# Performance work log

Measured on AMD Instinct MI355X. Metric: run time of the kernel, lower is better.

## Reference

```python
import jax, jax.numpy as jnp
import numpy as np
from jax import lax

LN_EPS = 1e-5

def _expert_ffn_all(x, w1, b1, g_ln, b_ln, w2, b2):
    # x: [B,S,D]; w1: [E,D,F]; w2: [E,F,O]
    h = jnp.einsum('bsd,edf->bsef', x, w1) + b1[None, None]          # [B,S,E,F]
    h = jax.nn.gelu(h, approximate=False)                            # torch default GELU (erf)
    mu = jnp.mean(h, axis=-1, keepdims=True)
    var = jnp.var(h, axis=-1, keepdims=True)
    h = (h - mu) / jnp.sqrt(var + LN_EPS) * g_ln[None, None] + b_ln[None, None]
    return jnp.einsum('bsef,efo->bseo', h, w2) + b2[None, None]      # [B,S,E,O]

def _moe_forward(x, w_gate, w1, b1, g_ln, b_ln, w2, b2):
    B, S, D = x.shape
    E = w_gate.shape[1]
    k = max(1, S // E)  # capacity_factor=1.0
    logits = jnp.einsum('bsd,de->bse', x, w_gate)                    # x_gated [B,S,E]
    probs = jax.nn.softmax(logits, axis=-1)
    # expert-choice top-k along the sequence dim of the raw logits
    _, idx = lax.top_k(jnp.transpose(logits, (0, 2, 1)), k)          # [B,E,k]
    b_ix = jnp.arange(B)[:, None, None]
    e_ix = jnp.arange(E)[None, :, None]
    mask_t = jnp.zeros((B, E, S), dtype=probs.dtype).at[b_ix, e_ix, idx].set(1.0)
    gate_scores = probs * jnp.transpose(mask_t, (0, 2, 1))           # [B,S,E]
    expert_out = _expert_ffn_all(x, w1, b1, g_ln, b_ln, w2, b2)      # [B,S,E,O]
    moe_output = jnp.einsum('bse,bseo->bso', gate_scores, expert_out)
    return moe_output, logits

def setup_inputs() -> dict:
    key = jax.random.key(0)
    ks = jax.random.split(key, 4)
    B, S, D, F, O, E = 2, 2048, 1024, 2048, 1024, 8
    sc1 = 1.0 / np.sqrt(D)
    sc2 = 1.0 / np.sqrt(F)
    return {
        'x': jax.random.normal(ks[0], (B, S, D), jnp.float32),
        'w_gate': jax.random.normal(ks[1], (D, E), jnp.float32) * sc1,
        'w1': jax.random.normal(ks[2], (E, D, F), jnp.float32) * sc1,
        'b1': jnp.zeros((E, F), jnp.float32),
        'g_ln': jnp.ones((E, F), jnp.float32),
        'b_ln': jnp.zeros((E, F), jnp.float32),
        'w2': jax.random.normal(ks[3], (E, F, O), jnp.float32) * sc2,
        'b2': jnp.zeros((E, O), jnp.float32),
    }

def reference(x, w_gate, w1, b1, g_ln, b_ln, w2, b2):
    return _moe_forward(x, w_gate, w1, b1, g_ln, b_ln, w2, b2)
```

## Files before the change

kernel.cpp:

```cpp
#include <hip/hip_runtime.h>
#include <cstdint>
#include <cstddef>

typedef __attribute__((ext_vector_type(8))) short bf16x8;
typedef __attribute__((ext_vector_type(4))) float f32x4;

#define S_    2048
#define D_    1024
#define F_    2048
#define O_    1024
#define E_    8
#define KCAP  256
#define ROWS  512
#define NTOK  4096

#define BK 64

__device__ __forceinline__ unsigned short f2bf(float f) {
  unsigned int u = __float_as_uint(f);
  u = (u + 0x7fffu + ((u >> 16) & 1u)) >> 16;
  return (unsigned short)u;
}
__device__ __forceinline__ float bf2f(unsigned short h) {
  return __uint_as_float(((unsigned int)h) << 16);
}

__device__ __forceinline__ void gload16(void* lds, const void* g) {
  auto gp = (__attribute__((address_space(1))) unsigned int*)(uintptr_t)g;
  auto lp = (__attribute__((address_space(3))) unsigned int*)(unsigned int)(uintptr_t)lds;
  __builtin_amdgcn_global_load_lds(gp, lp, 16, 0, 0);
}

__global__ void gating_kernel(const float* __restrict__ x, const float* __restrict__ wg,
                              float* __restrict__ logits, float* __restrict__ probs,
                              unsigned short* __restrict__ xb) {
  const int wave = threadIdx.x >> 6, lane = threadIdx.x & 63;
  const int t = blockIdx.x * 4 + wave;
  const float* xr = x + (size_t)t * D_;
  double acc[8] = {0, 0, 0, 0, 0, 0, 0, 0};
  const int d0 = lane * 16;
#pragma unroll
  for (int i = 0; i < 4; i++) {
    float4 xv = *(const float4*)&xr[d0 + i * 4];
    union { ushort4 u4; unsigned short u[4]; } cv;
    cv.u[0] = f2bf(xv.x); cv.u[1] = f2bf(xv.y); cv.u[2] = f2bf(xv.z); cv.u[3] = f2bf(xv.w);
    *(ushort4*)&xb[(size_t)t * D_ + d0 + i * 4] = cv.u4;
    float xs[4] = {xv.x, xv.y, xv.z, xv.w};
#pragma unroll
    for (int j = 0; j < 4; j++) {
      const float4* wr = (const float4*)&wg[(size_t)(d0 + i * 4 + j) * 8];
      float4 w0 = wr[0], w1v = wr[1];
      double xd = (double)xs[j];
      acc[0] += xd * (double)w0.x;  acc[1] += xd * (double)w0.y;
      acc[2] += xd * (double)w0.z;  acc[3] += xd * (double)w0.w;
      acc[4] += xd * (double)w1v.x; acc[5] += xd * (double)w1v.y;
      acc[6] += xd * (double)w1v.z; acc[7] += xd * (double)w1v.w;
    }
  }
#pragma unroll
  for (int off = 32; off; off >>= 1) {
#pragma unroll
    for (int e = 0; e < 8; e++) acc[e] += __shfl_down(acc[e], off);
  }
  if (lane == 0) {
    double m = acc[0];
    for (int e = 1; e < 8; e++) m = acc[e] > m ? acc[e] : m;
    double p[8]; double s = 0;
    for (int e = 0; e < 8; e++) { p[e] = exp(acc[e] - m); s += p[e]; }
    const double inv = 1.0 / s;
    for (int e = 0; e < 8; e++) {
      logits[(size_t)t * 8 + e] = (float)acc[e];
      probs [(size_t)t * 8 + e] = (float)(p[e] * inv);
    }
  }
}

__global__ void transpose_cvt_kernel(const float* __restrict__ in, unsigned short* __restrict__ out,
                                     const int R, const int C) {
  __shared__ float t[64][65];
  const int e = blockIdx.z;
  const float* inp = in + (size_t)e * R * C;
  unsigned short* outp = out + (size_t)e * R * C;
  const int r0 = blockIdx.y * 64, c0 = blockIdx.x * 64;
  const int tid = threadIdx.x;
  const int lr = tid >> 4;
  const int lc = (tid & 15) * 4;
#pragma unroll
  for (int i = 0; i < 4; i++) {
    const int r = lr + i * 16;
    const float4 v = *(const float4*)&inp[(size_t)(r0 + r) * C + c0 + lc];
    t[r][lc] = v.x; t[r][lc + 1] = v.y; t[r][lc + 2] = v.z; t[r][lc + 3] = v.w;
  }
  __syncthreads();
#pragma unroll
  for (int i = 0; i < 4; i++) {
    const int oc = lr + i * 16;
    union { ushort4 u4; unsigned short u[4]; } u;
#pragma unroll
    for (int j = 0; j < 4; j++) u.u[j] = f2bf(t[lc + j][oc]);
    *(ushort4*)&outp[(size_t)(c0 + oc) * R + r0 + lc] = u.u4;
  }
}

__global__ void topk_kernel(const float* __restrict__ logits, const float* __restrict__ probs,
                            int* __restrict__ sel, float* __restrict__ gate) {
  __shared__ unsigned int keys[S_];
  const int idx = blockIdx.x;
  const int seg = idx & 7;
  const int be = idx >> 3;
  const int b = be >> 3;
  const int e = be & 7;
  const int tid = threadIdx.x;
  for (int i = tid; i < S_; i += 256) {
    unsigned int u = __float_as_uint(logits[((size_t)(b * S_ + i)) * E_ + e]);
    keys[i] = u ^ ((u & 0x80000000u) ? 0xFFFFFFFFu : 0x80000000u);
  }
  __syncthreads();
  const int s = seg * 256 + tid;
  const unsigned int vk = keys[s];
  const int wave = tid >> 6;
  const int W0 = seg * 256 + wave * 64;
  int rank = 0;
#pragma unroll 4
  for (int i = 0; i < W0; i += 4) {
    const uint4 kv = *(const uint4*)&keys[i];
    rank += (kv.x >= vk) + (kv.y >= vk) + (kv.z >= vk) + (kv.w >= vk);
  }
#pragma unroll
  for (int j = 0; j < 64; j++) {
    const int i = W0 + j;
    const unsigned int kv = keys[i];
    rank += (kv > vk) || (kv == vk && i < s);
  }
#pragma unroll 4
  for (int i = W0 + 64; i < S_; i += 4) {
    const uint4 kv = *(const uint4*)&keys[i];
    rank += (kv.x > vk) + (kv.y > vk) + (kv.z > vk) + (kv.w > vk);
  }
  if (rank < KCAP) {
    sel [e * ROWS + b * KCAP + rank] = b * S_ + s;
    gate[e * ROWS + b * KCAP + rank] = probs[((size_t)(b * S_ + s)) * E_ + e];
  }
}

__global__ __launch_bounds__(512, 4) void gemm1_kernel(
    const unsigned short* __restrict__ xb,
    const unsigned short* __restrict__ w1t,
    const float* __restrict__ b1,
    const int* __restrict__ sel,
    unsigned short* __restrict__ hbuf) {
  __shared__ unsigned short As[2][128 * 64];
  __shared__ unsigned short Bs[2][128 * 64];
  const int bid = blockIdx.x;
  const int lid = (bid & 7) * 64 + (bid >> 3);
  const int e   = lid >> 6;
  const int rem = lid & 63;
  const int m0  = (rem & 3) * 128;
  const int n0  = (rem >> 2) * 128;
  const int tid = threadIdx.x;
  const int wave = tid >> 6, lane = tid & 63;
  const int wrow = wave >> 2;
  const int wcol = wave & 3;

  const int srow = tid >> 3;
  const int schunk = ((tid & 7) ^ (srow & 7)) * 8;
  const unsigned short* a0 = xb + (size_t)sel[e * ROWS + m0 + srow] * D_ + schunk;
  const unsigned short* a1 = xb + (size_t)sel[e * ROWS + m0 + srow + 64] * D_ + schunk;
  const unsigned short* b0 = w1t + ((size_t)e * F_ + n0 + srow) * D_ + schunk;
  const unsigned short* b1p = w1t + ((size_t)e * F_ + n0 + srow + 64) * D_ + schunk;
  const int ldst0 = wave * 512;
  const int ldst1 = 4096 + wave * 512;

  f32x4 acc[4][2];
#pragma unroll
  for (int mi = 0; mi < 4; mi++)
#pragma unroll
    for (int nj = 0; nj < 2; nj++) acc[mi][nj] = (f32x4){0.f, 0.f, 0.f, 0.f};

  auto stage = [&](int buf, int t) {
    const int k0 = t * BK;
    gload16(&As[buf][ldst0], a0 + k0);
    gload16(&As[buf][ldst1], a1 + k0);
    gload16(&Bs[buf][ldst0], b0 + k0);
    gload16(&Bs[buf][ldst1], b1p + k0);
  };
  const int fr = lane & 15;
  auto compute = [&](int buf) {
    const unsigned short* Ab = As[buf];
    const unsigned short* Bb = Bs[buf];
#pragma unroll
    for (int kk = 0; kk < 2; kk++) {
      const int q = kk * 4 + (lane >> 4);
      bf16x8 a[4], b[2];
#pragma unroll
      for (int mi = 0; mi < 4; mi++) {
        const int r = wrow * 64 + mi * 16 + fr;
        a[mi] = *(const bf16x8*)&Ab[r * 64 + ((q ^ (r & 7)) * 8)];
      }
#pragma unroll
      for (int nj = 0; nj < 2; nj++) {
        const int r = wcol * 32 + nj * 16 + fr;
        b[nj] = *(const bf16x8*)&Bb[r * 64 + ((q ^ (r & 7)) * 8)];
      }
#pragma unroll
      for (int mi = 0; mi < 4; mi++)
#pragma unroll
        for (int nj = 0; nj < 2; nj++)
          acc[mi][nj] = __builtin_amdgcn_mfma_f32_16x16x32_bf16(a[mi], b[nj], acc[mi][nj], 0, 0, 0);
    }
  };

  const int NT = D_ / BK;
  stage(0, 0);
  stage(1, 1);
  for (int t = 0; t < NT; t++) {
    if (t < NT - 1) asm volatile("s_waitcnt vmcnt(4)" ::: "memory");
    else            asm volatile("s_waitcnt vmcnt(0)" ::: "memory");
    asm volatile("s_barrier" ::: "memory");
    compute(t & 1);
    if (t + 2 < NT) {
      asm volatile("s_barrier" ::: "memory");
      stage(t & 1, t + 2);
    }
  }

#pragma unroll
  for (int mi = 0; mi < 4; mi++)
#pragma unroll
    for (int nj = 0; nj < 2; nj++)
#pragma unroll
      for (int rg = 0; rg < 4; rg++) {
        const int row = m0 + wrow * 64 + mi * 16 + (lane >> 4) * 4 + rg;
        const int col = n0 + wcol * 32 + nj * 16 + fr;
        float v = acc[mi][nj][rg] + b1[e * F_ + col];
        v = 0.5f * v * (1.0f + erff(v * 0.70710678118654752f));
        hbuf[((size_t)e * ROWS + row) * F_ + col] = f2bf(v);
      }
}

__global__ void ln_kernel(unsigned short* __restrict__ hbuf,
                          const float* __restrict__ g_ln, const float* __restrict__ b_ln) {
  const int row = blockIdx.x;
  const int e = row >> 9;
  unsigned short* hr = hbuf + (size_t)row * F_;
  const int tid = threadIdx.x;
  union { bf16x8 v; unsigned short u[8]; } u;
  u.v = *(const bf16x8*)&hr[tid * 8];
  float vals[8]; float s1 = 0.f, s2 = 0.f;
#pragma unroll
  for (int j = 0; j < 8; j++) { float f = bf2f(u.u[j]); vals[j] = f; s1 += f; s2 += f * f; }
#pragma unroll
  for (int off = 32; off; off >>= 1) { s1 += __shfl_down(s1, off); s2 += __shfl_down(s2, off); }
  __shared__ float rs[8];
  const int wave = tid >> 6, lane = tid & 63;
  if (lane == 0) { rs[wave] = s1; rs[wave + 4] = s2; }
  __syncthreads();
  const float t1 = rs[0] + rs[1] + rs[2] + rs[3];
  const float t2 = rs[4] + rs[5] + rs[6] + rs[7];
  const float mu = t1 * (1.f / F_);
  const float var = t2 * (1.f / F_) - mu * mu;
  const float rstd = rsqrtf(var + 1e-5f);
  const float4* gl4 = (const float4*)(g_ln + (size_t)e * F_ + tid * 8);
  const float4* bl4 = (const float4*)(b_ln + (size_t)e * F_ + tid * 8);
  float4 g0 = gl4[0], g1 = gl4[1], bb0 = bl4[0], bb1 = bl4[1];
  float gs[8] = {g0.x, g0.y, g0.z, g0.w, g1.x, g1.y, g1.z, g1.w};
  float bs[8] = {bb0.x, bb0.y, bb0.z, bb0.w, bb1.x, bb1.y, bb1.z, bb1.w};
  union { bf16x8 v; unsigned short u[8]; } o;
#pragma unroll
  for (int j = 0; j < 8; j++)
    o.u[j] = f2bf((vals[j] - mu) * rstd * gs[j] + bs[j]);
  *(bf16x8*)&hr[tid * 8] = o.v;
}

__global__ __launch_bounds__(512, 4) void gemm2_kernel(
    const unsigned short* __restrict__ hbuf,
    const unsigned short* __restrict__ w2t,
    const float* __restrict__ b2,
    const int* __restrict__ sel, const float* __restrict__ gate,
    float* __restrict__ out) {
  __shared__ unsigned short As[2][128 * 64];
  __shared__ unsigned short Bs[2][128 * 64];
  const int bid = blockIdx.x;
  const int lid = (bid & 7) * 64 + (bid >> 3);
  const int e   = lid >> 6;
  const int rem = lid & 63;
  const int khalf = rem & 1;
  const int m0  = ((rem >> 1) & 3) * 128;
  const int n0  = (rem >> 3) * 128;
  const int koff = khalf * (F_ / 2);
  const int tid = threadIdx.x;
  const int wave = tid >> 6, lane = tid & 63;
  const int wrow = wave >> 2;
  const int wcol = wave & 3;

  const int srow = tid >> 3;
  const int schunk = ((tid & 7) ^ (srow & 7)) * 8;
  const unsigned short* a0 = hbuf + ((size_t)e * ROWS + m0 + srow) * F_ + koff + schunk;
  const unsigned short* a1 = hbuf + ((size_t)e * ROWS + m0 + srow + 64) * F_ + koff + schunk;
  const unsigned short* b0 = w2t + ((size_t)e * O_ + n0 + srow) * F_ + koff + schunk;
  const unsigned short* b1p = w2t + ((size_t)e * O_ + n0 + srow + 64) * F_ + koff + schunk;
  const int ldst0 = wave * 512;
  const int ldst1 = 4096 + wave * 512;

  f32x4 acc[4][2];
#pragma unroll
  for (int mi = 0; mi < 4; mi++)
#pragma unroll
    for (int nj = 0; nj < 2; nj++) acc[mi][nj] = (f32x4){0.f, 0.f, 0.f, 0.f};

  auto stage = [&](int buf, int t) {
    const int k0 = t * BK;
    gload16(&As[buf][ldst0], a0 + k0);
    gload16(&As[buf][ldst1], a1 + k0);
    gload16(&Bs[buf][ldst0], b0 + k0);
    gload16(&Bs[buf][ldst1], b1p + k0);
  };
  const int fr = lane & 15;
  auto compute = [&](int buf) {
    const unsigned short* Ab = As[buf];
    const unsigned short* Bb = Bs[buf];
#pragma unroll
    for (int kk = 0; kk < 2; kk++) {
      const int q = kk * 4 + (lane >> 4);
      bf16x8 a[4], b[2];
#pragma unroll
      for (int mi = 0; mi < 4; mi++) {
        const int r = wrow * 64 + mi * 16 + fr;
        a[mi] = *(const bf16x8*)&Ab[r * 64 + ((q ^ (r & 7)) * 8)];
      }
#pragma unroll
      for (int nj = 0; nj < 2; nj++) {
        const int r = wcol * 32 + nj * 16 + fr;
        b[nj] = *(const bf16x8*)&Bb[r * 64 + ((q ^ (r & 7)) * 8)];
      }
#pragma unroll
      for (int mi = 0; mi < 4; mi++)
#pragma unroll
        for (int nj = 0; nj < 2; nj++)
          acc[mi][nj] = __builtin_amdgcn_mfma_f32_16x16x32_bf16(a[mi], b[nj], acc[mi][nj], 0, 0, 0);
    }
  };

  const int NT = (F_ / 2) / BK;
  stage(0, 0);
  stage(1, 1);
  for (int t = 0; t < NT; t++) {
    if (t < NT - 1) asm volatile("s_waitcnt vmcnt(4)" ::: "memory");
    else            asm volatile("s_waitcnt vmcnt(0)" ::: "memory");
    asm volatile("s_barrier" ::: "memory");
    compute(t & 1);
    if (t + 2 < NT) {
      asm volatile("s_barrier" ::: "memory");
      stage(t & 1, t + 2);
    }
  }

#pragma unroll
  for (int mi = 0; mi < 4; mi++) {
#pragma unroll
    for (int rg = 0; rg < 4; rg++) {
      const int row = m0 + wrow * 64 + mi * 16 + (lane >> 4) * 4 + rg;
      const int tok = sel[e * ROWS + row];
      const float g = gate[e * ROWS + row];
#pragma unroll
      for (int nj = 0; nj < 2; nj++) {
        const int col = n0 + wcol * 32 + nj * 16 + fr;
        float v = acc[mi][nj][rg];
        if (khalf == 0) v += b2[e * O_ + col];
        atomicAdd(&out[(size_t)tok * O_ + col], g * v);
      }
    }
  }
}

extern "C" void kernel_launch(void* const* d_in, const int* in_sizes, int n_in,
                              void* d_out, int out_size, void* d_ws, size_t ws_size,
                              hipStream_t stream) {
  const float* x     = (const float*)d_in[0];
  const float* wg    = (const float*)d_in[1];
  const float* w1    = (const float*)d_in[2];
  const float* b1    = (const float*)d_in[3];
  const float* g_ln  = (const float*)d_in[4];
  const float* b_ln  = (const float*)d_in[5];
  const float* w2    = (const float*)d_in[6];
  const float* b2    = (const float*)d_in[7];
  float* out = (float*)d_out;
  float* out_logits = out + (size_t)NTOK * O_;

  char* wsb = (char*)d_ws;
  unsigned short* xb   = (unsigned short*)(wsb + 0);
  unsigned short* w1t  = (unsigned short*)(wsb + 8388608);
  unsigned short* w2t  = (unsigned short*)(wsb + 41943040);
  unsigned short* hbuf = (unsigned short*)(wsb + 75497472);
  float* probs = (float*)(wsb + 92274688);
  int*   sel   = (int*)  (wsb + 92405760);
  float* gate  = (float*)(wsb + 92422144);

  hipMemsetAsync(d_out, 0, (size_t)NTOK * O_ * sizeof(float), stream);

  gating_kernel<<<NTOK / 4, 256, 0, stream>>>(x, wg, out_logits, probs, xb);
  transpose_cvt_kernel<<<dim3(F_ / 64, D_ / 64, E_), 256, 0, stream>>>(w1, w1t, D_, F_);
  transpose_cvt_kernel<<<dim3(O_ / 64, F_ / 64, E_), 256, 0, stream>>>(w2, w2t, F_, O_);
  topk_kernel<<<2 * E_ * 8, 256, 0, stream>>>(out_logits, probs, sel, gate);
  gemm1_kernel<<<512, 512, 0, stream>>>(xb, w1t, b1, sel, hbuf);
  ln_kernel<<<E_ * ROWS, 256, 0, stream>>>(hbuf, g_ln, b_ln);
  gemm2_kernel<<<512, 512, 0, stream>>>(hbuf, w2t, b2, sel, gate, out);
}
```

Baseline: 162.7 us.

## Load GEMM B operand directly into registers and shrink tiles to 64x128

```diff
diff --git a/kernel.cpp b/kernel.cpp
--- a/kernel.cpp
+++ b/kernel.cpp
@@ -143,33 +143,32 @@
   }
 }
 
-__global__ __launch_bounds__(512, 4) void gemm1_kernel(
+__global__ __launch_bounds__(256, 4) void gemm1_kernel(
     const unsigned short* __restrict__ xb,
     const unsigned short* __restrict__ w1t,
     const float* __restrict__ b1,
     const int* __restrict__ sel,
     unsigned short* __restrict__ hbuf) {
-  __shared__ unsigned short As[2][128 * 64];
-  __shared__ unsigned short Bs[2][128 * 64];
+  __shared__ unsigned short As[2][64 * 64];
   const int bid = blockIdx.x;
-  const int lid = (bid & 7) * 64 + (bid >> 3);
-  const int e   = lid >> 6;
-  const int rem = lid & 63;
-  const int m0  = (rem & 3) * 128;
-  const int n0  = (rem >> 2) * 128;
+  const int lid = (bid & 7) * 128 + (bid >> 3);
+  const int e   = lid >> 7;
+  const int rem = lid & 127;
+  const int m0  = (rem & 7) * 64;
+  const int n0  = (rem >> 3) * 128;
   const int tid = threadIdx.x;
   const int wave = tid >> 6, lane = tid & 63;
-  const int wrow = wave >> 2;
-  const int wcol = wave & 3;
-
-  const int srow = tid >> 3;
-  const int schunk = ((tid & 7) ^ (srow & 7)) * 8;
-  const unsigned short* a0 = xb + (size_t)sel[e * ROWS + m0 + srow] * D_ + schunk;
-  const unsigned short* a1 = xb + (size_t)sel[e * ROWS + m0 + srow + 64] * D_ + schunk;
-  const unsigned short* b0 = w1t + ((size_t)e * F_ + n0 + srow) * D_ + schunk;
-  const unsigned short* b1p = w1t + ((size_t)e * F_ + n0 + srow + 64) * D_ + schunk;
-  const int ldst0 = wave * 512;
-  const int ldst1 = 4096 + wave * 512;
+  const int fr = lane & 15;
+  const int kq = lane >> 4;
+
+  const unsigned short* a_src[2];
+#pragma unroll
+  for (int j = 0; j < 2; j++) {
+    const int r = wave * 16 + j * 8 + (lane >> 3);
+    const int chunk = (lane & 7) ^ (r & 7);
+    a_src[j] = xb + (size_t)sel[e * ROWS + m0 + r] * D_ + chunk * 8;
+  }
+  const unsigned short* bptr = w1t + ((size_t)(e * F_ + n0 + wave * 32 + fr)) * D_ + kq * 8;
 
   f32x4 acc[4][2];
 #pragma unroll
@@ -177,50 +176,54 @@
 #pragma unroll
     for (int nj = 0; nj < 2; nj++) acc[mi][nj] = (f32x4){0.f, 0.f, 0.f, 0.f};
 
-  auto stage = [&](int buf, int t) {
+  bf16x8 breg[2][2][2];
+
+  auto stageA = [&](int buf, int t) {
     const int k0 = t * BK;
-    gload16(&As[buf][ldst0], a0 + k0);
-    gload16(&As[buf][ldst1], a1 + k0);
-    gload16(&Bs[buf][ldst0], b0 + k0);
-    gload16(&Bs[buf][ldst1], b1p + k0);
-  };
-  const int fr = lane & 15;
-  auto compute = [&](int buf) {
-    const unsigned short* Ab = As[buf];
-    const unsigned short* Bb = Bs[buf];
+    gload16(&As[buf][(wave * 16 + 0) * 64], a_src[0] + k0);
+    gload16(&As[buf][(wave * 16 + 8) * 64], a_src[1] + k0);
+  };
+  auto loadB = [&](int buf, int t) {
+    const size_t k0 = (size_t)t * BK;
+#pragma unroll
+    for (int kk = 0; kk < 2; kk++)
+#pragma unroll
+      for (int nj = 0; nj < 2; nj++)
+        breg[buf][kk][nj] = *(const bf16x8*)(bptr + (size_t)nj * 16 * D_ + k0 + kk * 32);
+  };
+  auto compute = [&](int abuf, int bbuf) {
+    const unsigned short* Ab = As[abuf];
 #pragma unroll
     for (int kk = 0; kk < 2; kk++) {
-      const int q = kk * 4 + (lane >> 4);
-      bf16x8 a[4], b[2];
+      const int q = kk * 4 + kq;
+      bf16x8 a[4];
 #pragma unroll
       for (int mi = 0; mi < 4; mi++) {
-        const int r = wrow * 64 + mi * 16 + fr;
+        const int r = mi * 16 + fr;
         a[mi] = *(const bf16x8*)&Ab[r * 64 + ((q ^ (r & 7)) * 8)];
       }
 #pragma unroll
-      for (int nj = 0; nj < 2; nj++) {
-        const int r = wcol * 32 + nj * 16 + fr;
-        b[nj] = *(const bf16x8*)&Bb[r * 64 + ((q ^ (r & 7)) * 8)];
-      }
-#pragma unroll
       for (int mi = 0; mi < 4; mi++)
 #pragma unroll
         for (int nj = 0; nj < 2; nj++)
-          acc[mi][nj] = __builtin_amdgcn_mfma_f32_16x16x32_bf16(a[mi], b[nj], acc[mi][nj], 0, 0, 0);
+          acc[mi][nj] = __builtin_amdgcn_mfma_f32_16x16x32_bf16(a[mi], breg[bbuf][kk][nj], acc[mi][nj], 0, 0, 0);
     }
   };
 
   const int NT = D_ / BK;
-  stage(0, 0);
-  stage(1, 1);
+  stageA(0, 0);
+  stageA(1, 1);
+  loadB(0, 0);
+#pragma unroll 2
   for (int t = 0; t < NT; t++) {
-    if (t < NT - 1) asm volatile("s_waitcnt vmcnt(4)" ::: "memory");
-    else            asm volatile("s_waitcnt vmcnt(0)" ::: "memory");
+    if (t + 1 < NT) loadB((t + 1) & 1, t + 1);
+    if (t < NT - 1) asm volatile("s_waitcnt vmcnt(10)" ::: "memory");
+    else            asm volatile("s_waitcnt vmcnt(4)"  ::: "memory");
     asm volatile("s_barrier" ::: "memory");
-    compute(t & 1);
+    compute(t & 1, t & 1);
     if (t + 2 < NT) {
       asm volatile("s_barrier" ::: "memory");
-      stage(t & 1, t + 2);
+      stageA(t & 1, t + 2);
     }
   }
 
@@ -230,8 +233,8 @@
     for (int nj = 0; nj < 2; nj++)
 #pragma unroll
       for (int rg = 0; rg < 4; rg++) {
-        const int row = m0 + wrow * 64 + mi * 16 + (lane >> 4) * 4 + rg;
-        const int col = n0 + wcol * 32 + nj * 16 + fr;
+        const int row = m0 + mi * 16 + (lane >> 4) * 4 + rg;
+        const int col = n0 + wave * 32 + nj * 16 + fr;
         float v = acc[mi][nj][rg] + b1[e * F_ + col];
         v = 0.5f * v * (1.0f + erff(v * 0.70710678118654752f));
         hbuf[((size_t)e * ROWS + row) * F_ + col] = f2bf(v);
@@ -272,35 +275,34 @@
   *(bf16x8*)&hr[tid * 8] = o.v;
 }
 
-__global__ __launch_bounds__(512, 4) void gemm2_kernel(
+__global__ __launch_bounds__(256, 4) void gemm2_kernel(
     const unsigned short* __restrict__ hbuf,
     const unsigned short* __restrict__ w2t,
     const float* __restrict__ b2,
     const int* __restrict__ sel, const float* __restrict__ gate,
     float* __restrict__ out) {
-  __shared__ unsigned short As[2][128 * 64];
-  __shared__ unsigned short Bs[2][128 * 64];
+  __shared__ unsigned short As[2][64 * 64];
   const int bid = blockIdx.x;
-  const int lid = (bid & 7) * 64 + (bid >> 3);
-  const int e   = lid >> 6;
-  const int rem = lid & 63;
-  const int khalf = rem & 1;
-  const int m0  = ((rem >> 1) & 3) * 128;
-  const int n0  = (rem >> 3) * 128;
-  const int koff = khalf * (F_ / 2);
+  const int lid = (bid & 7) * 128 + (bid >> 3);
+  const int e     = lid >> 7;
+  const int rem   = lid & 127;
+  const int m0    = (rem & 7) * 64;
+  const int n0    = ((rem >> 3) & 7) * 128;
+  const int khalf = (rem >> 6) & 1;
+  const int koff  = khalf * (F_ / 2);
   const int tid = threadIdx.x;
   const int wave = tid >> 6, lane = tid & 63;
-  const int wrow = wave >> 2;
-  const int wcol = wave & 3;
-
-  const int srow = tid >> 3;
-  const int schunk = ((tid & 7) ^ (srow & 7)) * 8;
-  const unsigned short* a0 = hbuf + ((size_t)e * ROWS + m0 + srow) * F_ + koff + schunk;
-  const unsigned short* a1 = hbuf + ((size_t)e * ROWS + m0 + srow + 64) * F_ + koff + schunk;
-  const unsigned short* b0 = w2t + ((size_t)e * O_ + n0 + srow) * F_ + koff + schunk;
-  const unsigned short* b1p = w2t + ((size_t)e * O_ + n0 + srow + 64) * F_ + koff + schunk;
-  const int ldst0 = wave * 512;
-  const int ldst1 = 4096 + wave * 512;
+  const int fr = lane & 15;
+  const int kq = lane >> 4;
+
+  const unsigned short* a_src[2];
+#pragma unroll
+  for (int j = 0; j < 2; j++) {
+    const int r = wave * 16 + j * 8 + (lane >> 3);
+    const int chunk = (lane & 7) ^ (r & 7);
+    a_src[j] = hbuf + ((size_t)e * ROWS + m0 + r) * F_ + koff + chunk * 8;
+  }
+  const unsigned short* bptr = w2t + ((size_t)(e * O_ + n0 + wave * 32 + fr)) * F_ + koff + kq * 8;
 
   f32x4 acc[4][2];
 #pragma unroll
@@ -308,50 +310,54 @@
 #pragma unroll
     for (int nj = 0; nj < 2; nj++) acc[mi][nj] = (f32x4){0.f, 0.f, 0.f, 0.f};
 
-  auto stage = [&](int buf, int t) {
+  bf16x8 breg[2][2][2];
+
+  auto stageA = [&](int buf, int t) {
     const int k0 = t * BK;
-    gload16(&As[buf][ldst0], a0 + k0);
-    gload16(&As[buf][ldst1], a1 + k0);
-    gload16(&Bs[buf][ldst0], b0 + k0);
-    gload16(&Bs[buf][ldst1], b1p + k0);
-  };
-  const int fr = lane & 15;
-  auto compute = [&](int buf) {
-    const unsigned short* Ab = As[buf];
-    const unsigned short* Bb = Bs[buf];
+    gload16(&As[buf][(wave * 16 + 0) * 64], a_src[0] + k0);
+    gload16(&As[buf][(wave * 16 + 8) * 64], a_src[1] + k0);
+  };
+  auto loadB = [&](int buf, int t) {
+    const size_t k0 = (size_t)t * BK;
+#pragma unroll
+    for (int kk = 0; kk < 2; kk++)
+#pragma unroll
+      for (int nj = 0; nj < 2; nj++)
+        breg[buf][kk][nj] = *(const bf16x8*)(bptr + (size_t)nj * 16 * F_ + k0 + kk * 32);
+  };
+  auto compute = [&](int abuf, int bbuf) {
+    const unsigned short* Ab = As[abuf];
 #pragma unroll
     for (int kk = 0; kk < 2; kk++) {
-      const int q = kk * 4 + (lane >> 4);
-      bf16x8 a[4], b[2];
+      const int q = kk * 4 + kq;
+      bf16x8 a[4];
 #pragma unroll
       for (int mi = 0; mi < 4; mi++) {
-        const int r = wrow * 64 + mi * 16 + fr;
+        const int r = mi * 16 + fr;
         a[mi] = *(const bf16x8*)&Ab[r * 64 + ((q ^ (r & 7)) * 8)];
       }
 #pragma unroll
-      for (int nj = 0; nj < 2; nj++) {
-        const int r = wcol * 32 + nj * 16 + fr;
-        b[nj] = *(const bf16x8*)&Bb[r * 64 + ((q ^ (r & 7)) * 8)];
-      }
-#pragma unroll
       for (int mi = 0; mi < 4; mi++)
 #pragma unroll
         for (int nj = 0; nj < 2; nj++)
-          acc[mi][nj] = __builtin_amdgcn_mfma_f32_16x16x32_bf16(a[mi], b[nj], acc[mi][nj], 0, 0, 0);
+          acc[mi][nj] = __builtin_amdgcn_mfma_f32_16x16x32_bf16(a[mi], breg[bbuf][kk][nj], acc[mi][nj], 0, 0, 0);
     }
   };
 
   const int NT = (F_ / 2) / BK;
-  stage(0, 0);
-  stage(1, 1);
+  stageA(0, 0);
+  stageA(1, 1);
+  loadB(0, 0);
+#pragma unroll 2
   for (int t = 0; t < NT; t++) {
-    if (t < NT - 1) asm volatile("s_waitcnt vmcnt(4)" ::: "memory");
-    else            asm volatile("s_waitcnt vmcnt(0)" ::: "memory");
+    if (t + 1 < NT) loadB((t + 1) & 1, t + 1);
+    if (t < NT - 1) asm volatile("s_waitcnt vmcnt(10)" ::: "memory");
+    else            asm volatile("s_waitcnt vmcnt(4)"  ::: "memory");
     asm volatile("s_barrier" ::: "memory");
-    compute(t & 1);
+    compute(t & 1, t & 1);
     if (t + 2 < NT) {
       asm volatile("s_barrier" ::: "memory");
-      stage(t & 1, t + 2);
+      stageA(t & 1, t + 2);
     }
   }
 
@@ -359,12 +365,12 @@
   for (int mi = 0; mi < 4; mi++) {
 #pragma unroll
     for (int rg = 0; rg < 4; rg++) {
-      const int row = m0 + wrow * 64 + mi * 16 + (lane >> 4) * 4 + rg;
+      const int row = m0 + mi * 16 + (lane >> 4) * 4 + rg;
       const int tok = sel[e * ROWS + row];
       const float g = gate[e * ROWS + row];
 #pragma unroll
       for (int nj = 0; nj < 2; nj++) {
-        const int col = n0 + wcol * 32 + nj * 16 + fr;
+        const int col = n0 + wave * 32 + nj * 16 + fr;
         float v = acc[mi][nj][rg];
         if (khalf == 0) v += b2[e * O_ + col];
         atomicAdd(&out[(size_t)tok * O_ + col], g * v);
@@ -402,7 +408,7 @@
   transpose_cvt_kernel<<<dim3(F_ / 64, D_ / 64, E_), 256, 0, stream>>>(w1, w1t, D_, F_);
   transpose_cvt_kernel<<<dim3(O_ / 64, F_ / 64, E_), 256, 0, stream>>>(w2, w2t, F_, O_);
   topk_kernel<<<2 * E_ * 8, 256, 0, stream>>>(out_logits, probs, sel, gate);
-  gemm1_kernel<<<512, 512, 0, stream>>>(xb, w1t, b1, sel, hbuf);
+  gemm1_kernel<<<1024, 256, 0, stream>>>(xb, w1t, b1, sel, hbuf);
   ln_kernel<<<E_ * ROWS, 256, 0, stream>>>(hbuf, g_ln, b_ln);
-  gemm2_kernel<<<512, 512, 0, stream>>>(hbuf, w2t, b2, sel, gate, out);
-}
+  gemm2_kernel<<<1024, 256, 0, stream>>>(hbuf, w2t, b2, sel, gate, out);
+}
```

Measured after the change: 192.0 us. 18.0% more time.
